# Kernel optimization log

Measured on AMD Instinct MI355X. Metric: run time of the kernel, lower is better.

Reference implementation:

```python
import jax, jax.numpy as jnp
import numpy as np

S, D, M, K, H = 4096, 768, 1024, 32, 8
DH = D // H  # 96
CTX = 10
EPS_LN = 1e-5
EPS_COS = 1e-8


def setup_inputs() -> dict:
    key = jax.random.key(0)
    ks = jax.random.split(key, 30)
    sc = 0.02
    n = lambda k, shp: jax.random.normal(k, shp, jnp.float32) * sc
    inp = {
        "text_embeddings": jax.random.normal(ks[0], (1, S, D), jnp.float32),
        "candidate_embeddings": jax.random.normal(ks[1], (M, K, D), jnp.float32),
        "mention_starts": jax.random.randint(ks[2], (M,), 0, S - 16),
        "span_lengths": jax.random.randint(ks[3], (M,), 0, 8),
        # relik_reader: Linear(2D->D), ReLU, Linear(D->1)
        "relik_w1": n(ks[4], (2 * D, D)), "relik_b1": jnp.zeros((D,), jnp.float32),
        "relik_w2": n(ks[5], (D, 1)), "relik_b2": jnp.zeros((1,), jnp.float32),
        # TransformerEncoderLayer (post-norm, relu, nhead=8, ffn=4D)
        "wq": n(ks[6], (D, D)), "bq": jnp.zeros((D,), jnp.float32),
        "wk": n(ks[7], (D, D)), "bk": jnp.zeros((D,), jnp.float32),
        "wv": n(ks[8], (D, D)), "bv": jnp.zeros((D,), jnp.float32),
        "wo": n(ks[9], (D, D)), "bo": jnp.zeros((D,), jnp.float32),
        "ln1_g": jnp.ones((D,), jnp.float32), "ln1_b": jnp.zeros((D,), jnp.float32),
        "ffn_w1": n(ks[10], (D, 4 * D)), "ffn_b1": jnp.zeros((4 * D,), jnp.float32),
        "ffn_w2": n(ks[11], (4 * D, D)), "ffn_b2": jnp.zeros((D,), jnp.float32),
        "ln2_g": jnp.ones((D,), jnp.float32), "ln2_b": jnp.zeros((D,), jnp.float32),
        # unirel_interaction: Linear(2D->D), ReLU, Linear(D->D)
        "uni_w1": n(ks[12], (2 * D, D)), "uni_b1": jnp.zeros((D,), jnp.float32),
        "uni_w2": n(ks[13], (D, D)), "uni_b2": jnp.zeros((D,), jnp.float32),
    }
    return inp


def _ln(x, g, b):
    mu = jnp.mean(x, -1, keepdims=True)
    var = jnp.mean(jnp.square(x - mu), -1, keepdims=True)
    return (x - mu) * jax.lax.rsqrt(var + EPS_LN) * g + b


def reference(text_embeddings, candidate_embeddings, mention_starts, span_lengths,
              relik_w1, relik_b1, relik_w2, relik_b2,
              wq, bq, wk, bk, wv, bv, wo, bo,
              ln1_g, ln1_b, ffn_w1, ffn_b1, ffn_w2, ffn_b2, ln2_g, ln2_b,
              uni_w1, uni_b1, uni_w2, uni_b2):
    txt = text_embeddings[0]                               # [S, D]
    seq = txt.shape[0]
    csum = jnp.concatenate([jnp.zeros((1, txt.shape[1]), txt.dtype),
                            jnp.cumsum(txt, axis=0)], axis=0)  # [S+1, D]
    ends = mention_starts + span_lengths
    # mean over [start, end] inclusive
    m_len = (span_lengths + 1).astype(txt.dtype)
    mention = (csum[ends + 1] - csum[mention_starts]) / m_len[:, None]  # [M, D]
    # context mean over [c_start, c_end) exclusive, as in original slicing
    c_start = jnp.maximum(0, mention_starts - CTX)
    c_end = jnp.minimum(seq - 1, ends + CTX)
    ctx = (csum[c_end] - csum[c_start]) / (c_end - c_start).astype(txt.dtype)[:, None]

    cand = candidate_embeddings                            # [M, K, D]
    mk = jnp.broadcast_to(mention[:, None, :], cand.shape) # [M, K, D]

    # relik score: MLP on [mention; candidate]
    cat_mc = jnp.concatenate([mk, cand], axis=-1)          # [M, K, 2D]
    h = jax.nn.relu(cat_mc @ relik_w1 + relik_b1)
    relik = (h @ relik_w2 + relik_b2)[..., 0]              # [M, K]

    # 2-token transformer encoder layer over stack([mention, candidate])
    x = jnp.stack([mk, cand], axis=2)                      # [M, K, 2, D]
    q = (x @ wq + bq).reshape(M, K, 2, H, DH)
    k_ = (x @ wk + bk).reshape(M, K, 2, H, DH)
    v = (x @ wv + bv).reshape(M, K, 2, H, DH)
    scores = jnp.einsum("mkqhd,mkvhd->mkhqv", q, k_) / jnp.sqrt(jnp.float32(DH))
    attn = jax.nn.softmax(scores, axis=-1)
    o = jnp.einsum("mkhqv,mkvhd->mkqhd", attn, v).reshape(M, K, 2, D)
    x1 = _ln(x + (o @ wo + bo), ln1_g, ln1_b)
    f = jax.nn.relu(x1 @ ffn_w1 + ffn_b1) @ ffn_w2 + ffn_b2
    x2 = _ln(x1 + f, ln2_g, ln2_b)                         # [M, K, 2, D]
    e0, e1 = x2[..., 0, :], x2[..., 1, :]
    n0 = jnp.maximum(jnp.linalg.norm(e0, axis=-1), EPS_COS)
    n1 = jnp.maximum(jnp.linalg.norm(e1, axis=-1), EPS_COS)
    atg = jnp.sum(e0 * e1, axis=-1) / (n0 * n1)            # [M, K]

    # unirel: MLP on [context; candidate], sigmoid of mean
    ck = jnp.broadcast_to(ctx[:, None, :], cand.shape)
    cat_cc = jnp.concatenate([ck, cand], axis=-1)
    inter = jax.nn.relu(cat_cc @ uni_w1 + uni_b1) @ uni_w2 + uni_b2
    unirel = jax.nn.sigmoid(jnp.mean(inter, axis=-1))      # [M, K]

    return jnp.stack([relik, atg, unirel], axis=0)         # [3, M, K]
```

## Files before the change

### kernel.cpp

```cpp
#include <hip/hip_runtime.h>
#include <math.h>

#define S_LEN 4096
#define D_DIM 768
#define M_CNT 1024
#define K_CNT 32
#define MK_CNT 32768
#define DH_DIM 96
#define CTX_W 10

typedef __bf16 bf16_t;
typedef bf16_t bf16x8 __attribute__((ext_vector_type(8)));
typedef float f32x4 __attribute__((ext_vector_type(4)));
typedef float f32x16 __attribute__((ext_vector_type(16)));
typedef int i32x4 __attribute__((ext_vector_type(4)));
typedef int i32x8 __attribute__((ext_vector_type(8)));

__device__ __forceinline__ float block_reduce_sum(float v, float* sbuf) {
#pragma unroll
    for (int off = 32; off; off >>= 1) v += __shfl_down(v, off);
    __syncthreads();
    int wave = threadIdx.x >> 6;
    int lane = threadIdx.x & 63;
    if (lane == 0) sbuf[wave] = v;
    __syncthreads();
    return sbuf[0] + sbuf[1] + sbuf[2] + sbuf[3];
}

__device__ __forceinline__ float wave_sum(float v) {
#pragma unroll
    for (int off = 32; off; off >>= 1) v += __shfl_down(v, off);
    return __shfl(v, 0);
}

__device__ __forceinline__ unsigned char to_fp8(float v) {
    return (unsigned char)(__builtin_amdgcn_cvt_pk_fp8_f32(v, v, 0, false) & 0xff);
}

__device__ __forceinline__ void ld2(const bf16_t* p, float& a, float& b) {
    ushort2 u = *(const ushort2*)p;
    a = __uint_as_float((unsigned)u.x << 16);
    b = __uint_as_float((unsigned)u.y << 16);
}

template<int OUT_BF16, int RELU>
__global__ __launch_bounds__(256, 2) void gemm_mfma(
    const bf16_t* __restrict__ A, const bf16_t* __restrict__ Bt,
    const float* __restrict__ bias, void* __restrict__ C,
    int Kd, int N, int nx, int ny)
{
    __shared__ bf16_t As[128 * 64];
    __shared__ bf16_t Bs[128 * 64];
    const int tid = threadIdx.x;
    const int w = tid >> 6, l = tid & 63;
    int per = 8 * nx;
    int g = blockIdx.x / per, rr = blockIdx.x % per;
    int gs = ny - g * 8; if (gs > 8) gs = 8;
    const int row0 = (g * 8 + rr % gs) * 128, col0 = (rr / gs) * 128;

    const int srow = w * 8 + (l >> 3);
    const int gchunk = (l & 7) ^ ((l >> 3) & 7);
    const bf16_t* gA = A + (size_t)(row0 + srow) * Kd + gchunk * 8;
    const bf16_t* gB = Bt + (size_t)(col0 + srow) * Kd + gchunk * 8;

    const int wm = w >> 1, wn = w & 1;
    f32x4 acc[4][4] = {};

    for (int k0 = 0; k0 < Kd; k0 += 64) {
#pragma unroll
        for (int c = 0; c < 4; ++c) {
            __builtin_amdgcn_global_load_lds(
                (const __attribute__((address_space(1))) void*)(gA + (size_t)(c * 32) * Kd + k0),
                (__attribute__((address_space(3))) void*)(As + (c * 256 + w * 64) * 8), 16, 0, 0);
            __builtin_amdgcn_global_load_lds(
                (const __attribute__((address_space(1))) void*)(gB + (size_t)(c * 32) * Kd + k0),
                (__attribute__((address_space(3))) void*)(Bs + (c * 256 + w * 64) * 8), 16, 0, 0);
        }
        __syncthreads();
#pragma unroll
        for (int ks = 0; ks < 2; ++ks) {
            bf16x8 af[4], bfr[4];
#pragma unroll
            for (int i = 0; i < 4; ++i) {
                int arow = wm * 64 + i * 16 + (l & 15);
                int slot = (ks * 4 + (l >> 4)) ^ (l & 7);
                af[i] = *(const bf16x8*)(As + arow * 64 + slot * 8);
                int brow = wn * 64 + i * 16 + (l & 15);
                bfr[i] = *(const bf16x8*)(Bs + brow * 64 + slot * 8);
            }
#pragma unroll
            for (int i = 0; i < 4; ++i)
#pragma unroll
                for (int j = 0; j < 4; ++j)
                    acc[i][j] = __builtin_amdgcn_mfma_f32_16x16x32_bf16(af[i], bfr[j], acc[i][j], 0, 0, 0);
        }
        __syncthreads();
    }

#pragma unroll
    for (int i = 0; i < 4; ++i) {
        int row = row0 + wm * 64 + i * 16 + (l >> 4) * 4;
#pragma unroll
        for (int j = 0; j < 4; ++j) {
            int col = col0 + wn * 64 + j * 16 + (l & 15);
            float bv = bias ? bias[col] : 0.f;
#pragma unroll
            for (int r = 0; r < 4; ++r) {
                float v = acc[i][j][r] + bv;
                if (RELU) v = fmaxf(v, 0.f);
                if (OUT_BF16) ((bf16_t*)C)[(size_t)(row + r) * N + col] = (bf16_t)v;
                else          ((float*)C)[(size_t)(row + r) * N + col] = v;
            }
        }
    }
}

static inline void launch_gemm(const bf16_t* A, const bf16_t* Bt, const float* bias, void* C,
                               int rows, int Kd, int N, bool relu, bool outbf, hipStream_t st) {
    int nx = N / 128, ny = rows / 128;
    dim3 grid(nx * ny);
    if (outbf) {
        if (relu) gemm_mfma<1, 1><<<grid, 256, 0, st>>>(A, Bt, bias, C, Kd, N, nx, ny);
        else      gemm_mfma<1, 0><<<grid, 256, 0, st>>>(A, Bt, bias, C, Kd, N, nx, ny);
    } else {
        if (relu) gemm_mfma<0, 1><<<grid, 256, 0, st>>>(A, Bt, bias, C, Kd, N, nx, ny);
        else      gemm_mfma<0, 0><<<grid, 256, 0, st>>>(A, Bt, bias, C, Kd, N, nx, ny);
    }
}

template<int OMODE, int RELU, int RESID>
__global__ __launch_bounds__(256, 2) void gemm_fp8(
    const unsigned char* __restrict__ A, const unsigned char* __restrict__ Bt,
    const float* __restrict__ bias, void* __restrict__ C,
    const bf16_t* __restrict__ resid,
    int Kd, int N, int nx, int ny)
{
    __shared__ unsigned char As[256 * 128];
    __shared__ unsigned char Bs[128 * 128];
    const int tid = threadIdx.x;
    const int w = tid >> 6, l = tid & 63;
    int per = 8 * nx;
    int g = blockIdx.x / per, rrb = blockIdx.x % per;
    int gs = ny - g * 8; if (gs > 8) gs = 8;
    const int row0 = (g * 8 + rrb % gs) * 256, col0 = (rrb / gs) * 128;
    const int wm = w >> 1, wn = w & 1;
    const int SA = 0x7F7F7F7F;

    const int srow = w * 8 + (l >> 3);
    const int gch = (l & 7) ^ ((l >> 3) & 7);
    const unsigned char* gA = A + (size_t)(row0 + srow) * Kd + gch * 16;
    const unsigned char* gB = Bt + (size_t)(col0 + srow) * Kd + gch * 16;

    f32x16 acc[4][2] = {};

    for (int k0 = 0; k0 < Kd; k0 += 128) {
#pragma unroll
        for (int q = 0; q < 8; ++q)
            __builtin_amdgcn_global_load_lds(
                (const __attribute__((address_space(1))) void*)(gA + (size_t)(q * 32) * Kd + k0),
                (__attribute__((address_space(3))) void*)(As + (q * 256 + w * 64) * 16), 16, 0, 0);
#pragma unroll
        for (int q = 0; q < 4; ++q)
            __builtin_amdgcn_global_load_lds(
                (const __attribute__((address_space(1))) void*)(gB + (size_t)(q * 32) * Kd + k0),
                (__attribute__((address_space(3))) void*)(Bs + (q * 256 + w * 64) * 16), 16, 0, 0);
        __syncthreads();
#pragma unroll
        for (int s = 0; s < 2; ++s) {
            int cb = s * 4 + ((l >> 5) << 1);
            i32x8 af[4], bfr[2];
#pragma unroll
            for (int i = 0; i < 4; ++i) {
                int row = wm * 128 + i * 32 + (l & 31);
                int sl0 = cb ^ (row & 7);
                int sl1 = (cb + 1) ^ (row & 7);
                i32x4 lo = *(const i32x4*)(As + (row * 8 + sl0) * 16);
                i32x4 hi = *(const i32x4*)(As + (row * 8 + sl1) * 16);
                i32x8 a;
                a[0] = lo[0]; a[1] = lo[1]; a[2] = lo[2]; a[3] = lo[3];
                a[4] = hi[0]; a[5] = hi[1]; a[6] = hi[2]; a[7] = hi[3];
                af[i] = a;
            }
#pragma unroll
            for (int j = 0; j < 2; ++j) {
                int colr = wn * 64 + j * 32 + (l & 31);
                int tl0 = cb ^ (colr & 7);
                int tl1 = (cb + 1) ^ (colr & 7);
                i32x4 lo = *(const i32x4*)(Bs + (colr * 8 + tl0) * 16);
                i32x4 hi = *(const i32x4*)(Bs + (colr * 8 + tl1) * 16);
                i32x8 b;
                b[0] = lo[0]; b[1] = lo[1]; b[2] = lo[2]; b[3] = lo[3];
                b[4] = hi[0]; b[5] = hi[1]; b[6] = hi[2]; b[7] = hi[3];
                bfr[j] = b;
            }
#pragma unroll
            for (int i = 0; i < 4; ++i)
#pragma unroll
                for (int j = 0; j < 2; ++j)
                    acc[i][j] = __builtin_amdgcn_mfma_scale_f32_32x32x64_f8f6f4(
                        af[i], bfr[j], acc[i][j], 0, 0, 0, SA, 0, SA);
        }
        __syncthreads();
    }

#pragma unroll
    for (int i = 0; i < 4; ++i) {
        int rbase = row0 + wm * 128 + i * 32 + 4 * (l >> 5);
#pragma unroll
        for (int j = 0; j < 2; ++j) {
            int col = col0 + wn * 64 + j * 32 + (l & 31);
            float bv = bias ? bias[col] : 0.f;
#pragma unroll
            for (int reg = 0; reg < 16; ++reg) {
                int row = rbase + (reg & 3) + 8 * (reg >> 2);
                float v = acc[i][j][reg] + bv;
                if (RESID) v += (float)resid[(size_t)row * N + col];
                if (RELU) v = fmaxf(v, 0.f);
                if (OMODE == 1)
                    ((unsigned char*)C)[(size_t)row * N + col] = to_fp8(v);
                else if (OMODE == 2)
                    ((bf16_t*)C)[(size_t)row * N + col] = (bf16_t)v;
                else
                    ((float*)C)[(size_t)row * N + col] = v;
            }
        }
    }
}

template<int OMODE, int RELU, int RESID>
static inline void launch_fp8_t(const unsigned char* A, const unsigned char* Bt, const float* bias,
                                void* C, const bf16_t* resid, int rows, int Kd, int N, hipStream_t st) {
    int nx = N / 128, ny = rows / 256;
    gemm_fp8<OMODE, RELU, RESID><<<dim3(nx * ny), 256, 0, st>>>(A, Bt, bias, C, resid, Kd, N, nx, ny);
}

__global__ __launch_bounds__(256) void transpose_bf16(
    const float* __restrict__ W, bf16_t* __restrict__ Wt, int Kd, int N)
{
    __shared__ float t[32][33];
    int bx = blockIdx.x * 32, by = blockIdx.y * 32;
    int x = threadIdx.x & 31, y = threadIdx.x >> 5;
#pragma unroll
    for (int yy = y; yy < 32; yy += 8) t[yy][x] = W[(size_t)(by + yy) * N + bx + x];
    __syncthreads();
#pragma unroll
    for (int yy = y; yy < 32; yy += 8) Wt[(size_t)(bx + yy) * Kd + by + x] = (bf16_t)t[x][yy];
}

__global__ __launch_bounds__(256) void transpose_fp8(
    const float* __restrict__ W, unsigned char* __restrict__ Wt, int Kd, int N)
{
    __shared__ float t[32][33];
    int bx = blockIdx.x * 32, by = blockIdx.y * 32;
    int x = threadIdx.x & 31, y = threadIdx.x >> 5;
#pragma unroll
    for (int yy = y; yy < 32; yy += 8) t[yy][x] = W[(size_t)(by + yy) * N + bx + x];
    __syncthreads();
    int xg = threadIdx.x & 7, yo = threadIdx.x >> 3;
    int lo = __builtin_amdgcn_cvt_pk_fp8_f32(t[xg * 4 + 0][yo], t[xg * 4 + 1][yo], 0, false);
    int both = __builtin_amdgcn_cvt_pk_fp8_f32(t[xg * 4 + 2][yo], t[xg * 4 + 3][yo], lo, true);
    *(int*)(Wt + (size_t)(bx + yo) * Kd + by + xg * 4) = both;
}

__global__ __launch_bounds__(256) void cvt_cand(
    const float* __restrict__ x, bf16_t* __restrict__ yb,
    unsigned char* __restrict__ yq, int n4)
{
    int i = blockIdx.x * 256 + threadIdx.x;
    if (i < n4) {
        float4 v = ((const float4*)x)[i];
        bf16_t o4[4] = {(bf16_t)v.x, (bf16_t)v.y, (bf16_t)v.z, (bf16_t)v.w};
        ((uint2*)yb)[i] = *(uint2*)o4;
        int lo = __builtin_amdgcn_cvt_pk_fp8_f32(v.x, v.y, 0, false);
        int both = __builtin_amdgcn_cvt_pk_fp8_f32(v.z, v.w, lo, true);
        ((int*)yq)[i] = both;
    }
}

__global__ __launch_bounds__(256) void pack_bias(
    const float* __restrict__ bq, const float* __restrict__ bk,
    const float* __restrict__ bv, float* __restrict__ o)
{
    int i = blockIdx.x * 256 + threadIdx.x;
    if (i < 768) { o[i] = bq[i]; o[i + 768] = bk[i]; o[i + 1536] = bv[i]; }
}

__global__ __launch_bounds__(256) void spans_kernel(
    const float* __restrict__ txt, const int* __restrict__ starts,
    const int* __restrict__ lens, float* __restrict__ mention,
    unsigned char* __restrict__ mentionq, bf16_t* __restrict__ mentionb,
    bf16_t* __restrict__ ctxb)
{
    int m = blockIdx.x;
    int st = starts[m], ln = lens[m];
    int en = st + ln;
    int cs = st - CTX_W; if (cs < 0) cs = 0;
    int ce = en + CTX_W; if (ce > S_LEN - 1) ce = S_LEN - 1;
    int c = threadIdx.x;
    float s0 = 0.f, s1 = 0.f, s2 = 0.f;
    for (int r = st; r <= en; ++r) {
        const float* tr = txt + (size_t)r * D_DIM;
        s0 += tr[c]; s1 += tr[c + 256]; s2 += tr[c + 512];
    }
    float inv = 1.f / (float)(ln + 1);
    float v0 = s0 * inv, v1 = s1 * inv, v2 = s2 * inv;
    float* mp = mention + (size_t)m * D_DIM;
    bf16_t* mb = mentionb + (size_t)m * D_DIM;
    unsigned char* mq = mentionq + (size_t)m * D_DIM;
    mp[c] = v0; mp[c + 256] = v1; mp[c + 512] = v2;
    mb[c] = (bf16_t)v0; mb[c + 256] = (bf16_t)v1; mb[c + 512] = (bf16_t)v2;
    mq[c] = to_fp8(v0); mq[c + 256] = to_fp8(v1); mq[c + 512] = to_fp8(v2);

    s0 = 0.f; s1 = 0.f; s2 = 0.f;
    for (int r = cs; r < ce; ++r) {
        const float* tr = txt + (size_t)r * D_DIM;
        s0 += tr[c]; s1 += tr[c + 256]; s2 += tr[c + 512];
    }
    inv = 1.f / (float)(ce - cs);
    bf16_t* cp = ctxb + (size_t)m * D_DIM;
    cp[c] = (bf16_t)(s0 * inv); cp[c + 256] = (bf16_t)(s1 * inv); cp[c + 512] = (bf16_t)(s2 * inv);
}

__global__ __launch_bounds__(256) void w2bar_kernel(
    const float* __restrict__ uni_w2, const float* __restrict__ uni_b2,
    float* __restrict__ w2bar, float* __restrict__ b2bar)
{
    __shared__ float sbuf[4];
    int d = blockIdx.x;
    float s = 0.f;
    if (d < D_DIM) {
        for (int j = threadIdx.x; j < D_DIM; j += 256) s += uni_w2[(size_t)d * D_DIM + j];
        s = block_reduce_sum(s, sbuf);
        if (threadIdx.x == 0) w2bar[d] = s * (1.f / (float)D_DIM);
    } else {
        for (int j = threadIdx.x; j < D_DIM; j += 256) s += uni_b2[j];
        s = block_reduce_sum(s, sbuf);
        if (threadIdx.x == 0) *b2bar = s * (1.f / (float)D_DIM);
    }
}

__global__ __launch_bounds__(512) void attn_kernel(
    const bf16_t* __restrict__ qkvm, const bf16_t* __restrict__ qkvc,
    unsigned char* __restrict__ o, int g0)
{
    int lc = blockIdx.x;
    int gg = g0 + lc;
    int m = gg >> 5;
    int h = threadIdx.x >> 6;
    int lane = threadIdx.x & 63;
    const bf16_t* bm = qkvm + (size_t)m * 2304 + h * DH_DIM;
    const bf16_t* bc = qkvc + (size_t)lc * 2304 + h * DH_DIM;

    float s00 = 0.f, s01 = 0.f, s10 = 0.f, s11 = 0.f;
    int d = lane * 2;
    if (lane < 48) {
        float qm0, qm1, km0, km1, qc0, qc1, kc0, kc1;
        ld2(bm + d, qm0, qm1);
        ld2(bm + 768 + d, km0, km1);
        ld2(bc + d, qc0, qc1);
        ld2(bc + 768 + d, kc0, kc1);
        s00 = qm0 * km0 + qm1 * km1;
        s01 = qm0 * kc0 + qm1 * kc1;
        s10 = qc0 * km0 + qc1 * km1;
        s11 = qc0 * kc0 + qc1 * kc1;
    }
#pragma unroll
    for (int off = 32; off; off >>= 1) {
        s00 += __shfl_down(s00, off); s01 += __shfl_down(s01, off);
        s10 += __shfl_down(s10, off); s11 += __shfl_down(s11, off);
    }
    s00 = __shfl(s00, 0); s01 = __shfl(s01, 0);
    s10 = __shfl(s10, 0); s11 = __shfl(s11, 0);
    const float sc = 0.1020620726159658f;
    s00 *= sc; s01 *= sc; s10 *= sc; s11 *= sc;
    float m0 = fmaxf(s00, s01), m1 = fmaxf(s10, s11);
    float e00 = expf(s00 - m0), e01 = expf(s01 - m0);
    float e10 = expf(s10 - m1), e11 = expf(s11 - m1);
    float i0 = 1.f / (e00 + e01), i1 = 1.f / (e10 + e11);
    float a00 = e00 * i0, a01 = e01 * i0, a10 = e10 * i1, a11 = e11 * i1;

    unsigned char* o0 = o + ((size_t)lc * 2) * D_DIM + h * DH_DIM;
    unsigned char* o1 = o0 + D_DIM;
    if (lane < 48) {
        float vm0, vm1, vc0, vc1;
        ld2(bm + 1536 + d, vm0, vm1);
        ld2(bc + 1536 + d, vc0, vc1);
        unsigned r0 = __builtin_amdgcn_cvt_pk_fp8_f32(a00 * vm0 + a01 * vc0, a00 * vm1 + a01 * vc1, 0, false);
        unsigned r1 = __builtin_amdgcn_cvt_pk_fp8_f32(a10 * vm0 + a11 * vc0, a10 * vm1 + a11 * vc1, 0, false);
        *(unsigned short*)(o0 + d) = (unsigned short)(r0 & 0xffff);
        *(unsigned short*)(o1 + d) = (unsigned short)(r1 & 0xffff);
    }
}

__global__ __launch_bounds__(256) void ln1_kernel(
    const bf16_t* __restrict__ x1pre, const float* __restrict__ mention,
    const bf16_t* __restrict__ candb, const float* __restrict__ g,
    const float* __restrict__ b, bf16_t* __restrict__ x1f,
    unsigned char* __restrict__ x1q, int g0)
{
    int w = threadIdx.x >> 6, l = threadIdx.x & 63;
    int r = blockIdx.x * 4 + w;
    int lc = r >> 1, pos = r & 1;
    int gg = g0 + lc, m = gg >> 5;
    float v[12];
    const bf16_t* pr = x1pre + (size_t)r * D_DIM;
    if (pos) {
        const bf16_t* xr = candb + (size_t)gg * D_DIM;
#pragma unroll
        for (int i = 0; i < 12; ++i) { int j = l + i * 64; v[i] = (float)xr[j] + (float)pr[j]; }
    } else {
        const float* xr = mention + (size_t)m * D_DIM;
#pragma unroll
        for (int i = 0; i < 12; ++i) { int j = l + i * 64; v[i] = xr[j] + (float)pr[j]; }
    }
    float s = 0.f;
#pragma unroll
    for (int i = 0; i < 12; ++i) s += v[i];
    float mu = wave_sum(s) * (1.f / (float)D_DIM);
    float vv = 0.f;
#pragma unroll
    for (int i = 0; i < 12; ++i) { float d = v[i] - mu; vv += d * d; }
    float var = wave_sum(vv) * (1.f / (float)D_DIM);
    float inv = rsqrtf(var + 1e-5f);
    bf16_t* fp = x1f + (size_t)r * D_DIM;
    unsigned char* qp = x1q + (size_t)r * D_DIM;
#pragma unroll
    for (int i = 0; i < 12; ++i) {
        int j = l + i * 64;
        float o = (v[i] - mu) * inv * g[j] + b[j];
        fp[j] = (bf16_t)o;
        qp[j] = to_fp8(o);
    }
}

__global__ __launch_bounds__(256) void heads_kernel(
    const bf16_t* __restrict__ y,
    const float* __restrict__ g2, const float* __restrict__ b2g,
    const float* __restrict__ Ar, const float* __restrict__ Au,
    const bf16_t* __restrict__ ru, const float* __restrict__ rw2,
    const float* __restrict__ rb2, const float* __restrict__ w2bar,
    const float* __restrict__ b2bar, float* __restrict__ out, int g0)
{
    int w = threadIdx.x >> 6, l = threadIdx.x & 63;
    int lc = blockIdx.x * 4 + w;
    int gg = g0 + lc, m = gg >> 5;
    const bf16_t* y0 = y + (size_t)(2 * lc) * D_DIM;
    const bf16_t* y1 = y0 + D_DIM;
    float v0[12], v1[12];
    float s0 = 0.f, s1 = 0.f;
#pragma unroll
    for (int i = 0; i < 12; ++i) {
        int j = l + i * 64;
        v0[i] = (float)y0[j]; v1[i] = (float)y1[j];
        s0 += v0[i]; s1 += v1[i];
    }
    float mu0 = wave_sum(s0) * (1.f / (float)D_DIM);
    float mu1 = wave_sum(s1) * (1.f / (float)D_DIM);
    float q0 = 0.f, q1 = 0.f;
#pragma unroll
    for (int i = 0; i < 12; ++i) {
        float d0 = v0[i] - mu0, d1 = v1[i] - mu1;
        q0 += d0 * d0; q1 += d1 * d1;
    }
    float inv0 = rsqrtf(wave_sum(q0) * (1.f / (float)D_DIM) + 1e-5f);
    float inv1 = rsqrtf(wave_sum(q1) * (1.f / (float)D_DIM) + 1e-5f);

    const float* ar = Ar + (size_t)m * D_DIM;
    const float* au = Au + (size_t)m * D_DIM;
    const bf16_t* br = ru + (size_t)lc * 1536;
    const bf16_t* bu = br + 768;

    float dd = 0.f, aa = 0.f, bb = 0.f, rs = 0.f, us = 0.f;
#pragma unroll
    for (int i = 0; i < 12; ++i) {
        int j = l + i * 64;
        float e0 = (v0[i] - mu0) * inv0 * g2[j] + b2g[j];
        float e1 = (v1[i] - mu1) * inv1 * g2[j] + b2g[j];
        dd += e0 * e1; aa += e0 * e0; bb += e1 * e1;
        rs += fmaxf(ar[j] + (float)br[j], 0.f) * rw2[j];
        us += fmaxf(au[j] + (float)bu[j], 0.f) * w2bar[j];
    }
    dd = wave_sum(dd); aa = wave_sum(aa); bb = wave_sum(bb);
    rs = wave_sum(rs); us = wave_sum(us);
    if (l == 0) {
        float n0 = fmaxf(sqrtf(aa), 1e-8f);
        float n1 = fmaxf(sqrtf(bb), 1e-8f);
        out[MK_CNT + gg] = dd / (n0 * n1);
        out[gg] = rs + rb2[0];
        float z = us + *b2bar;
        out[2 * MK_CNT + gg] = 1.f / (1.f + expf(-z));
    }
}

extern "C" void kernel_launch(void* const* d_in, const int* in_sizes, int n_in,
                              void* d_out, int out_size, void* d_ws, size_t ws_size,
                              hipStream_t stream) {
    const float* text     = (const float*)d_in[0];
    const float* cand     = (const float*)d_in[1];
    const int*   starts   = (const int*)d_in[2];
    const int*   lens     = (const int*)d_in[3];
    const float* relik_w1 = (const float*)d_in[4];
    const float* relik_b1 = (const float*)d_in[5];
    const float* relik_w2 = (const float*)d_in[6];
    const float* relik_b2 = (const float*)d_in[7];
    const float* wq = (const float*)d_in[8];
    const float* bq = (const float*)d_in[9];
    const float* wk = (const float*)d_in[10];
    const float* bk = (const float*)d_in[11];
    const float* wv = (const float*)d_in[12];
    const float* bv = (const float*)d_in[13];
    const float* wo = (const float*)d_in[14];
    const float* bo = (const float*)d_in[15];
    const float* ln1_g = (const float*)d_in[16];
    const float* ln1_b = (const float*)d_in[17];
    const float* ffn_w1 = (const float*)d_in[18];
    const float* ffn_b1 = (const float*)d_in[19];
    const float* ffn_w2 = (const float*)d_in[20];
    const float* ffn_b2 = (const float*)d_in[21];
    const float* ln2_g = (const float*)d_in[22];
    const float* ln2_b = (const float*)d_in[23];
    const float* uni_w1 = (const float*)d_in[24];
    const float* uni_b1 = (const float*)d_in[25];
    const float* uni_w2 = (const float*)d_in[26];
    const float* uni_b2 = (const float*)d_in[27];
    float* out = (float*)d_out;

    const size_t MD = (size_t)M_CNT * D_DIM;
    const size_t DD = (size_t)D_DIM * D_DIM;

    size_t fixed_f = 26500000;
    int NC = 32768;
    while (NC > 256 && (fixed_f + (size_t)NC * 4224) * 4 > ws_size) NC >>= 1;
    const size_t NCD = (size_t)NC * D_DIM;

    float* p = (float*)d_ws;
    float* mention = p; p += MD;
    float* Ar      = p; p += MD;
    float* Au      = p; p += MD;
    float* bqkv    = p; p += 2304;
    float* w2bar   = p; p += 768;
    float* b2bar   = p; p += 64;
    bf16_t* mentionb = (bf16_t*)p; p += MD / 2;
    bf16_t* ctxb     = (bf16_t*)p; p += MD / 2;
    unsigned char* mentionq = (unsigned char*)p; p += MD / 4;
    bf16_t* qkvm     = (bf16_t*)p; p += (size_t)M_CNT * 2304 / 2;
    bf16_t* relikAT  = (bf16_t*)p; p += DD / 2;
    bf16_t* uniAT    = (bf16_t*)p; p += DD / 2;
    bf16_t* wruT     = (bf16_t*)p; p += 2 * DD / 2;
    unsigned char* wqkvq = (unsigned char*)p; p += 3 * DD / 4;
    unsigned char* woq   = (unsigned char*)p; p += DD / 4;
    unsigned char* w1q = (unsigned char*)p; p += (size_t)3072 * 768 / 4;
    unsigned char* w2q = (unsigned char*)p; p += (size_t)3072 * 768 / 4;
    bf16_t* candb    = (bf16_t*)p; p += (size_t)MK_CNT * D_DIM / 2;
    unsigned char* candq = (unsigned char*)p; p += (size_t)MK_CNT * D_DIM / 4;

    bf16_t* qkvcb = (bf16_t*)p;
    bf16_t* x1f   = (bf16_t*)p;
    unsigned char* x1q = (unsigned char*)(x1f + 2 * NCD);
    p += (size_t)NC * 2304 / 2;
    bf16_t* rucb  = (bf16_t*)p; p += (size_t)NC * 1536 / 2;
    bf16_t* x1pre = (bf16_t*)p;
    bf16_t* x2f   = x1pre;
    p += NCD;
    unsigned char* hb   = (unsigned char*)p;
    unsigned char* obuf = hb;
    p += (size_t)NC * 1536;

    dim3 t768(768 / 32, 768 / 32);
    transpose_fp8<<<t768, 256, 0, stream>>>(wq, wqkvq, 768, 768);
    transpose_fp8<<<t768, 256, 0, stream>>>(wk, wqkvq + DD, 768, 768);
    transpose_fp8<<<t768, 256, 0, stream>>>(wv, wqkvq + 2 * DD, 768, 768);
    transpose_fp8<<<t768, 256, 0, stream>>>(wo, woq, 768, 768);
    transpose_bf16<<<t768, 256, 0, stream>>>(relik_w1 + DD, wruT, 768, 768);
    transpose_bf16<<<t768, 256, 0, stream>>>(uni_w1 + DD, wruT + DD, 768, 768);
    transpose_bf16<<<t768, 256, 0, stream>>>(relik_w1, relikAT, 768, 768);
    transpose_bf16<<<t768, 256, 0, stream>>>(uni_w1, uniAT, 768, 768);
    transpose_fp8<<<dim3(3072 / 32, 768 / 32), 256, 0, stream>>>(ffn_w1, w1q, 768, 3072);
    transpose_fp8<<<dim3(768 / 32, 3072 / 32), 256, 0, stream>>>(ffn_w2, w2q, 3072, 768);
    pack_bias<<<3, 256, 0, stream>>>(bq, bk, bv, bqkv);
    w2bar_kernel<<<D_DIM + 1, 256, 0, stream>>>(uni_w2, uni_b2, w2bar, b2bar);
    cvt_cand<<<(MK_CNT * D_DIM / 4 + 255) / 256, 256, 0, stream>>>(cand, candb, candq, MK_CNT * D_DIM / 4);

    spans_kernel<<<M_CNT, 256, 0, stream>>>(text, starts, lens, mention, mentionq, mentionb, ctxb);
    launch_fp8_t<2, 0, 0>(mentionq, wqkvq, bqkv, qkvm, nullptr, M_CNT, 768, 2304, stream);
    launch_gemm(mentionb, relikAT, relik_b1, Ar, M_CNT, 768, 768, false, false, stream);
    launch_gemm(ctxb, uniAT, uni_b1, Au, M_CNT, 768, 768, false, false, stream);

    int nch = MK_CNT / NC;
    for (int c = 0; c < nch; ++c) {
        int g0 = c * NC;
        launch_fp8_t<2, 0, 0>(candq + (size_t)g0 * D_DIM, wqkvq, bqkv, qkvcb, nullptr, NC, 768, 2304, stream);
        launch_gemm(candb + (size_t)g0 * D_DIM, wruT, nullptr, rucb, NC, 768, 1536, false, true, stream);

        attn_kernel<<<NC, 512, 0, stream>>>(qkvm, qkvcb, obuf, g0);

        launch_fp8_t<2, 0, 0>(obuf, woq, bo, x1pre, nullptr, 2 * NC, 768, 768, stream);
        ln1_kernel<<<2 * NC / 4, 256, 0, stream>>>(x1pre, mention, candb,
                                                   ln1_g, ln1_b, x1f, x1q, g0);

        launch_fp8_t<1, 1, 0>(x1q, w1q, ffn_b1, hb, nullptr, 2 * NC, 768, 3072, stream);
        launch_fp8_t<2, 0, 1>(hb, w2q, ffn_b2, x2f, x1f, 2 * NC, 3072, 768, stream);

        heads_kernel<<<NC / 4, 256, 0, stream>>>(x2f, ln2_g, ln2_b, Ar, Au, rucb,
                                                 relik_w2, relik_b2, w2bar, b2bar, out, g0);
    }
}
```

Measured before the change: 1.177 ms.

## Double-buffer LDS tiles in FP8 GEMM with a smaller K step

Restructures the FP8 MFMA GEMM main loop to use two LDS buffers with a K-step of 64. It prefetches the next tile via global_load_lds while the current tile is being computed, and changes the swizzle to fit 64-byte rows. The aim is to overlap global-to-LDS loads with MFMA work instead of stalling at a barrier each iteration. In exchange it takes twice as many loop iterations, each with a barrier, and correctness depends on the new swizzle and the staging offsets matching.

After: 1.239 ms. 5.3% more time.

```diff
diff --git a/kernel.cpp b/kernel.cpp
--- a/kernel.cpp
+++ b/kernel.cpp
@@ -135,8 +135,8 @@
     const bf16_t* __restrict__ resid,
     int Kd, int N, int nx, int ny)
 {
-    __shared__ unsigned char As[256 * 128];
-    __shared__ unsigned char Bs[128 * 128];
+    __shared__ unsigned char As[2 * 256 * 64];
+    __shared__ unsigned char Bs[2 * 128 * 64];
     const int tid = threadIdx.x;
     const int w = tid >> 6, l = tid & 63;
     int per = 8 * nx;
@@ -146,60 +146,67 @@
     const int wm = w >> 1, wn = w & 1;
     const int SA = 0x7F7F7F7F;
 
-    const int srow = w * 8 + (l >> 3);
-    const int gch = (l & 7) ^ ((l >> 3) & 7);
-    const unsigned char* gA = A + (size_t)(row0 + srow) * Kd + gch * 16;
-    const unsigned char* gB = Bt + (size_t)(col0 + srow) * Kd + gch * 16;
+    const int srow = l >> 2;
+    const int gch = (l & 3) ^ ((l >> 3) & 3);
+    const unsigned char* gA = A + (size_t)(row0 + w * 64 + srow) * Kd + gch * 16;
+    const unsigned char* gB = Bt + (size_t)(col0 + w * 32 + srow) * Kd + gch * 16;
 
     f32x16 acc[4][2] = {};
-
-    for (int k0 = 0; k0 < Kd; k0 += 128) {
-#pragma unroll
-        for (int q = 0; q < 8; ++q)
+    const int nk = Kd >> 6;
+
+    auto stage = [&](int buf, int k0) {
+#pragma unroll
+        for (int c = 0; c < 4; ++c)
             __builtin_amdgcn_global_load_lds(
-                (const __attribute__((address_space(1))) void*)(gA + (size_t)(q * 32) * Kd + k0),
-                (__attribute__((address_space(3))) void*)(As + (q * 256 + w * 64) * 16), 16, 0, 0);
-#pragma unroll
-        for (int q = 0; q < 4; ++q)
+                (const __attribute__((address_space(1))) void*)(gA + (size_t)(c * 16) * Kd + k0),
+                (__attribute__((address_space(3))) void*)(As + buf * 16384 + (w * 64 + c * 16) * 64), 16, 0, 0);
+#pragma unroll
+        for (int c = 0; c < 2; ++c)
             __builtin_amdgcn_global_load_lds(
-                (const __attribute__((address_space(1))) void*)(gB + (size_t)(q * 32) * Kd + k0),
-                (__attribute__((address_space(3))) void*)(Bs + (q * 256 + w * 64) * 16), 16, 0, 0);
-        __syncthreads();
-#pragma unroll
-        for (int s = 0; s < 2; ++s) {
-            int cb = s * 4 + ((l >> 5) << 1);
-            i32x8 af[4], bfr[2];
-#pragma unroll
-            for (int i = 0; i < 4; ++i) {
-                int row = wm * 128 + i * 32 + (l & 31);
-                int sl0 = cb ^ (row & 7);
-                int sl1 = (cb + 1) ^ (row & 7);
-                i32x4 lo = *(const i32x4*)(As + (row * 8 + sl0) * 16);
-                i32x4 hi = *(const i32x4*)(As + (row * 8 + sl1) * 16);
-                i32x8 a;
-                a[0] = lo[0]; a[1] = lo[1]; a[2] = lo[2]; a[3] = lo[3];
-                a[4] = hi[0]; a[5] = hi[1]; a[6] = hi[2]; a[7] = hi[3];
-                af[i] = a;
-            }
-#pragma unroll
-            for (int j = 0; j < 2; ++j) {
-                int colr = wn * 64 + j * 32 + (l & 31);
-                int tl0 = cb ^ (colr & 7);
-                int tl1 = (cb + 1) ^ (colr & 7);
-                i32x4 lo = *(const i32x4*)(Bs + (colr * 8 + tl0) * 16);
-                i32x4 hi = *(const i32x4*)(Bs + (colr * 8 + tl1) * 16);
-                i32x8 b;
-                b[0] = lo[0]; b[1] = lo[1]; b[2] = lo[2]; b[3] = lo[3];
-                b[4] = hi[0]; b[5] = hi[1]; b[6] = hi[2]; b[7] = hi[3];
-                bfr[j] = b;
-            }
-#pragma unroll
-            for (int i = 0; i < 4; ++i)
-#pragma unroll
-                for (int j = 0; j < 2; ++j)
-                    acc[i][j] = __builtin_amdgcn_mfma_scale_f32_32x32x64_f8f6f4(
-                        af[i], bfr[j], acc[i][j], 0, 0, 0, SA, 0, SA);
+                (const __attribute__((address_space(1))) void*)(gB + (size_t)(c * 16) * Kd + k0),
+                (__attribute__((address_space(3))) void*)(Bs + buf * 8192 + (w * 32 + c * 16) * 64), 16, 0, 0);
+    };
+
+    stage(0, 0);
+    __syncthreads();
+
+    for (int t = 0; t < nk; ++t) {
+        const int cur = t & 1;
+        if (t + 1 < nk) stage(cur ^ 1, (t + 1) << 6);
+
+        const unsigned char* as = As + cur * 16384;
+        const unsigned char* bs = Bs + cur * 8192;
+        const int cb = (l >> 5) << 1;
+        i32x8 af[4], bfr[2];
+#pragma unroll
+        for (int i = 0; i < 4; ++i) {
+            int row = wm * 128 + i * 32 + (l & 31);
+            int sl0 = cb ^ ((row >> 1) & 3);
+            i32x4 lo = *(const i32x4*)(as + row * 64 + sl0 * 16);
+            i32x4 hi = *(const i32x4*)(as + row * 64 + (sl0 ^ 1) * 16);
+            i32x8 a;
+            a[0] = lo[0]; a[1] = lo[1]; a[2] = lo[2]; a[3] = lo[3];
+            a[4] = hi[0]; a[5] = hi[1]; a[6] = hi[2]; a[7] = hi[3];
+            af[i] = a;
         }
+#pragma unroll
+        for (int j = 0; j < 2; ++j) {
+            int colr = wn * 64 + j * 32 + (l & 31);
+            int tl0 = cb ^ ((colr >> 1) & 3);
+            i32x4 lo = *(const i32x4*)(bs + colr * 64 + tl0 * 16);
+            i32x4 hi = *(const i32x4*)(bs + colr * 64 + (tl0 ^ 1) * 16);
+            i32x8 b;
+            b[0] = lo[0]; b[1] = lo[1]; b[2] = lo[2]; b[3] = lo[3];
+            b[4] = hi[0]; b[5] = hi[1]; b[6] = hi[2]; b[7] = hi[3];
+            bfr[j] = b;
+        }
+#pragma unroll
+        for (int i = 0; i < 4; ++i)
+#pragma unroll
+            for (int j = 0; j < 2; ++j)
+                acc[i][j] = __builtin_amdgcn_mfma_scale_f32_32x32x64_f8f6f4(
+                    af[i], bfr[j], acc[i][j], 0, 0, 0, SA, 0, SA);
+
         __syncthreads();
     }
 
```

## Prepack fp8 weights into MFMA fragment order and load B directly to registers

Applied to the files above, without the earlier changes.

The fp8 weight transposes now write weights in a layout that matches the MFMA B-fragment order per 32-column group and K tile. The fp8 GEMM drops its B shared-memory tile and has each lane load its B fragments straight from global memory with coalesced 16-byte loads. This cuts LDS traffic and shared-memory footprint, which could allow higher occupancy. In exchange, B fragments are loaded redundantly by the waves that share a column group, and the global load latency is exposed before the MFMAs run.

New measurement: 1.186 ms. Within noise of the previous version (+0.8%).

```diff
diff --git a/kernel.cpp b/kernel.cpp
--- a/kernel.cpp
+++ b/kernel.cpp
@@ -130,13 +130,12 @@
 
 template<int OMODE, int RELU, int RESID>
 __global__ __launch_bounds__(256, 2) void gemm_fp8(
-    const unsigned char* __restrict__ A, const unsigned char* __restrict__ Bt,
+    const unsigned char* __restrict__ A, const unsigned char* __restrict__ Bp,
     const float* __restrict__ bias, void* __restrict__ C,
     const bf16_t* __restrict__ resid,
     int Kd, int N, int nx, int ny)
 {
     __shared__ unsigned char As[256 * 128];
-    __shared__ unsigned char Bs[128 * 128];
     const int tid = threadIdx.x;
     const int w = tid >> 6, l = tid & 63;
     int per = 8 * nx;
@@ -145,26 +144,38 @@
     const int row0 = (g * 8 + rrb % gs) * 256, col0 = (rrb / gs) * 128;
     const int wm = w >> 1, wn = w & 1;
     const int SA = 0x7F7F7F7F;
+    const int KT = Kd >> 7;
 
     const int srow = w * 8 + (l >> 3);
     const int gch = (l & 7) ^ ((l >> 3) & 7);
     const unsigned char* gA = A + (size_t)(row0 + srow) * Kd + gch * 16;
-    const unsigned char* gB = Bt + (size_t)(col0 + srow) * Kd + gch * 16;
+
+    const int cg0 = (col0 >> 5) + wn * 2;
+    const unsigned char* gB0 = Bp + (size_t)cg0 * KT * 4096 + (l >> 5) * 1024 + (l & 31) * 16;
+    const unsigned char* gB1 = gB0 + (size_t)KT * 4096;
 
     f32x16 acc[4][2] = {};
 
-    for (int k0 = 0; k0 < Kd; k0 += 128) {
+    for (int kt = 0; kt < KT; ++kt) {
 #pragma unroll
         for (int q = 0; q < 8; ++q)
             __builtin_amdgcn_global_load_lds(
-                (const __attribute__((address_space(1))) void*)(gA + (size_t)(q * 32) * Kd + k0),
+                (const __attribute__((address_space(1))) void*)(gA + (size_t)(q * 32) * Kd + kt * 128),
                 (__attribute__((address_space(3))) void*)(As + (q * 256 + w * 64) * 16), 16, 0, 0);
-#pragma unroll
-        for (int q = 0; q < 4; ++q)
-            __builtin_amdgcn_global_load_lds(
-                (const __attribute__((address_space(1))) void*)(gB + (size_t)(q * 32) * Kd + k0),
-                (__attribute__((address_space(3))) void*)(Bs + (q * 256 + w * 64) * 16), 16, 0, 0);
+
+        const unsigned char* p0 = gB0 + (size_t)kt * 4096;
+        const unsigned char* p1 = gB1 + (size_t)kt * 4096;
+        i32x4 b00l = *(const i32x4*)(p0);
+        i32x4 b00h = *(const i32x4*)(p0 + 512);
+        i32x4 b01l = *(const i32x4*)(p0 + 2048);
+        i32x4 b01h = *(const i32x4*)(p0 + 2560);
+        i32x4 b10l = *(const i32x4*)(p1);
+        i32x4 b10h = *(const i32x4*)(p1 + 512);
+        i32x4 b11l = *(const i32x4*)(p1 + 2048);
+        i32x4 b11h = *(const i32x4*)(p1 + 2560);
+
         __syncthreads();
+
 #pragma unroll
         for (int s = 0; s < 2; ++s) {
             int cb = s * 4 + ((l >> 5) << 1);
@@ -181,17 +192,18 @@
                 a[4] = hi[0]; a[5] = hi[1]; a[6] = hi[2]; a[7] = hi[3];
                 af[i] = a;
             }
-#pragma unroll
-            for (int j = 0; j < 2; ++j) {
-                int colr = wn * 64 + j * 32 + (l & 31);
-                int tl0 = cb ^ (colr & 7);
-                int tl1 = (cb + 1) ^ (colr & 7);
-                i32x4 lo = *(const i32x4*)(Bs + (colr * 8 + tl0) * 16);
-                i32x4 hi = *(const i32x4*)(Bs + (colr * 8 + tl1) * 16);
+            {
+                i32x4 lo = s ? b01l : b00l;
+                i32x4 hi = s ? b01h : b00h;
                 i32x8 b;
                 b[0] = lo[0]; b[1] = lo[1]; b[2] = lo[2]; b[3] = lo[3];
                 b[4] = hi[0]; b[5] = hi[1]; b[6] = hi[2]; b[7] = hi[3];
-                bfr[j] = b;
+                bfr[0] = b;
+                lo = s ? b11l : b10l;
+                hi = s ? b11h : b10h;
+                b[0] = lo[0]; b[1] = lo[1]; b[2] = lo[2]; b[3] = lo[3];
+                b[4] = hi[0]; b[5] = hi[1]; b[6] = hi[2]; b[7] = hi[3];
+                bfr[1] = b;
             }
 #pragma unroll
             for (int i = 0; i < 4; ++i)
@@ -228,10 +240,10 @@
 }
 
 template<int OMODE, int RELU, int RESID>
-static inline void launch_fp8_t(const unsigned char* A, const unsigned char* Bt, const float* bias,
+static inline void launch_fp8_t(const unsigned char* A, const unsigned char* Bp, const float* bias,
                                 void* C, const bf16_t* resid, int rows, int Kd, int N, hipStream_t st) {
     int nx = N / 128, ny = rows / 256;
-    gemm_fp8<OMODE, RELU, RESID><<<dim3(nx * ny), 256, 0, st>>>(A, Bt, bias, C, resid, Kd, N, nx, ny);
+    gemm_fp8<OMODE, RELU, RESID><<<dim3(nx * ny), 256, 0, st>>>(A, Bp, bias, C, resid, Kd, N, nx, ny);
 }
 
 __global__ __launch_bounds__(256) void transpose_bf16(
@@ -247,8 +259,8 @@
     for (int yy = y; yy < 32; yy += 8) Wt[(size_t)(bx + yy) * Kd + by + x] = (bf16_t)t[x][yy];
 }
 
-__global__ __launch_bounds__(256) void transpose_fp8(
-    const float* __restrict__ W, unsigned char* __restrict__ Wt, int Kd, int N)
+__global__ __launch_bounds__(256) void pack_fp8(
+    const float* __restrict__ W, unsigned char* __restrict__ P, int Kd, int N)
 {
     __shared__ float t[32][33];
     int bx = blockIdx.x * 32, by = blockIdx.y * 32;
@@ -259,7 +271,14 @@
     int xg = threadIdx.x & 7, yo = threadIdx.x >> 3;
     int lo = __builtin_amdgcn_cvt_pk_fp8_f32(t[xg * 4 + 0][yo], t[xg * 4 + 1][yo], 0, false);
     int both = __builtin_amdgcn_cvt_pk_fp8_f32(t[xg * 4 + 2][yo], t[xg * 4 + 3][yo], lo, true);
-    *(int*)(Wt + (size_t)(bx + yo) * Kd + by + xg * 4) = both;
+    int cg = blockIdx.x;
+    int kt = by >> 7;
+    int s = (by >> 6) & 1;
+    int half = (by >> 5) & 1;
+    int chunk = xg >> 2;
+    size_t off = (((size_t)cg * (Kd >> 7) + kt) * 4096) + s * 2048 + half * 1024
+               + chunk * 512 + yo * 16 + (xg & 3) * 4;
+    *(int*)(P + off) = both;
 }
 
 __global__ __launch_bounds__(256) void cvt_cand(
@@ -567,16 +586,16 @@
     p += (size_t)NC * 1536;
 
     dim3 t768(768 / 32, 768 / 32);
-    transpose_fp8<<<t768, 256, 0, stream>>>(wq, wqkvq, 768, 768);
-    transpose_fp8<<<t768, 256, 0, stream>>>(wk, wqkvq + DD, 768, 768);
-    transpose_fp8<<<t768, 256, 0, stream>>>(wv, wqkvq + 2 * DD, 768, 768);
-    transpose_fp8<<<t768, 256, 0, stream>>>(wo, woq, 768, 768);
+    pack_fp8<<<t768, 256, 0, stream>>>(wq, wqkvq, 768, 768);
+    pack_fp8<<<t768, 256, 0, stream>>>(wk, wqkvq + DD, 768, 768);
+    pack_fp8<<<t768, 256, 0, stream>>>(wv, wqkvq + 2 * DD, 768, 768);
+    pack_fp8<<<t768, 256, 0, stream>>>(wo, woq, 768, 768);
     transpose_bf16<<<t768, 256, 0, stream>>>(relik_w1 + DD, wruT, 768, 768);
     transpose_bf16<<<t768, 256, 0, stream>>>(uni_w1 + DD, wruT + DD, 768, 768);
     transpose_bf16<<<t768, 256, 0, stream>>>(relik_w1, relikAT, 768, 768);
     transpose_bf16<<<t768, 256, 0, stream>>>(uni_w1, uniAT, 768, 768);
-    transpose_fp8<<<dim3(3072 / 32, 768 / 32), 256, 0, stream>>>(ffn_w1, w1q, 768, 3072);
-    transpose_fp8<<<dim3(768 / 32, 3072 / 32), 256, 0, stream>>>(ffn_w2, w2q, 3072, 768);
+    pack_fp8<<<dim3(3072 / 32, 768 / 32), 256, 0, stream>>>(ffn_w1, w1q, 768, 3072);
+    pack_fp8<<<dim3(768 / 32, 3072 / 32), 256, 0, stream>>>(ffn_w2, w2q, 3072, 768);
     pack_bias<<<3, 256, 0, stream>>>(bq, bk, bv, bqkv);
     w2bar_kernel<<<D_DIM + 1, 256, 0, stream>>>(uni_w2, uni_b2, w2bar, b2bar);
     cvt_cand<<<(MK_CNT * D_DIM / 4 + 255) / 256, 256, 0, stream>>>(cand, candb, candq, MK_CNT * D_DIM / 4);
```
